# Kernel tuning notes

Hardware: AMD Instinct MI355X
Metric: run time of the kernel (lower is better)

The kernel has to match this reference:

```python
import jax, jax.numpy as jnp
import numpy as np

B, L, D = 16, 2048, 256

def setup_inputs() -> dict:
    key = jax.random.key(0)
    k1, k2 = jax.random.split(key)
    inp = jax.random.normal(k1, (B, L, D), dtype=jnp.float32)
    # Linear(2*dim, 1, bias=False) weight, torch layout [out=1, in=2*dim]
    v_w = jax.random.normal(k2, (1, 2 * D), dtype=jnp.float32) * (1.0 / np.sqrt(2 * D))
    return {"inp": inp, "v_w": v_w}


def reference(inp, v_w):
    # score[b,i,j] = cat(query=inp[b,i], key=inp[b,j]) . v_w
    # decomposes exactly into two rank-1 projections broadcast-summed.
    dim = inp.shape[-1]
    wq = v_w[0, :dim]   # multiplies the query half (unsqueeze(1) -> index i)
    wk = v_w[0, dim:]   # multiplies the key half (unsqueeze(2) -> index j)
    sq = jnp.einsum('bld,d->bl', inp, wq)          # [B,L]
    sk = jnp.einsum('bld,d->bl', inp, wk)          # [B,L]
    score = sq[:, :, None] + sk[:, None, :]        # [B,L,L]
    attn = jax.nn.softmax(score, axis=2)           # Softmax(2)
    out = jnp.einsum('bij,bjd->bid', attn, inp)    # bmm
    return (out, attn)
```

## Files before the change

kernel.cpp:

```cpp
#include <hip/hip_runtime.h>

#define BB 16
#define LL 2048
#define DD 256

__global__ void k1_sk(const float* __restrict__ inp, const float* __restrict__ wk,
                      float* __restrict__ sk) {
    int tid  = threadIdx.x;
    int wid  = tid >> 6, lane = tid & 63;
    int row  = blockIdx.x * 4 + wid;
    const float4 a = *reinterpret_cast<const float4*>(inp + (size_t)row * DD + lane * 4);
    const float4 w = *reinterpret_cast<const float4*>(wk + lane * 4);
    float dot = a.x * w.x + a.y * w.y + a.z * w.z + a.w * w.w;
    #pragma unroll
    for (int off = 32; off >= 1; off >>= 1) dot += __shfl_down(dot, off, 64);
    if (lane == 0) sk[row] = dot;
}

__global__ void k2_softmax(const float* __restrict__ sk, float* __restrict__ p) {
    int b = blockIdx.x;
    int tid = threadIdx.x;
    int lane = tid & 63, wid = tid >> 6;
    const float* skb = sk + b * LL;
    float v[8];
    #pragma unroll
    for (int r = 0; r < 8; ++r) v[r] = skb[tid + r * 256];
    float mx = v[0];
    #pragma unroll
    for (int r = 1; r < 8; ++r) mx = fmaxf(mx, v[r]);
    __shared__ float sm[4];
    __shared__ float bc;
    #pragma unroll
    for (int off = 32; off >= 1; off >>= 1) mx = fmaxf(mx, __shfl_down(mx, off, 64));
    if (lane == 0) sm[wid] = mx;
    __syncthreads();
    if (tid == 0) bc = fmaxf(fmaxf(sm[0], sm[1]), fmaxf(sm[2], sm[3]));
    __syncthreads();
    float m = bc;
    float e[8], s = 0.f;
    #pragma unroll
    for (int r = 0; r < 8; ++r) { e[r] = __expf(v[r] - m); s += e[r]; }
    #pragma unroll
    for (int off = 32; off >= 1; off >>= 1) s += __shfl_down(s, off, 64);
    __syncthreads();
    if (lane == 0) sm[wid] = s;
    __syncthreads();
    if (tid == 0) bc = (sm[0] + sm[1]) + (sm[2] + sm[3]);
    __syncthreads();
    float inv = 1.0f / bc;
    #pragma unroll
    for (int r = 0; r < 8; ++r) p[b * LL + tid + r * 256] = e[r] * inv;
}

__global__ void k3a_partial(const float* __restrict__ inp, const float* __restrict__ p,
                            float* __restrict__ partial) {
    int blk = blockIdx.x;
    int b = blk >> 4, jc = blk & 15;
    int t = threadIdx.x;
    const float* pb = p + b * LL + jc * 128;
    const float* ib = inp + ((size_t)(b * LL + jc * 128)) * DD + t;
    float acc = 0.f;
    #pragma unroll 4
    for (int j = 0; j < 128; ++j) acc += pb[j] * ib[(size_t)j * DD];
    partial[(size_t)blk * DD + t] = acc;
}

__global__ void k3b_reduce(const float* __restrict__ partial, float* __restrict__ out_vec) {
    int b = blockIdx.x;
    int t = threadIdx.x;
    float acc = 0.f;
    #pragma unroll
    for (int jc = 0; jc < 16; ++jc) acc += partial[((size_t)(b * 16 + jc)) * DD + t];
    out_vec[b * DD + t] = acc;
}

__global__ void k4_write(const float4* __restrict__ outv4, const float4* __restrict__ p4,
                         float4* __restrict__ dst) {
    const size_t OUT4 = (size_t)BB * LL * DD / 4;
    const size_t TOT4 = OUT4 + (size_t)BB * LL * LL / 4;
    size_t stride = (size_t)gridDim.x * blockDim.x;
    for (size_t i = blockIdx.x * (size_t)blockDim.x + threadIdx.x; i < TOT4; i += stride) {
        float4 v;
        if (i < OUT4) {
            size_t b  = i >> 17;
            size_t d4 = i & 63;
            v = outv4[(b << 6) + d4];
        } else {
            size_t k  = i - OUT4;
            size_t b  = k >> 20;
            size_t j4 = k & 511;
            v = p4[(b << 9) + j4];
        }
        dst[i] = v;
    }
}

extern "C" void kernel_launch(void* const* d_in, const int* in_sizes, int n_in,
                              void* d_out, int out_size, void* d_ws, size_t ws_size,
                              hipStream_t stream) {
    const float* inp = (const float*)d_in[0];
    const float* vw  = (const float*)d_in[1];
    float* out = (float*)d_out;
    float* ws  = (float*)d_ws;

    float* sk      = ws;
    float* p       = ws + 32768;
    float* partial = ws + 65536;
    float* out_vec = ws + 131072;

    k1_sk      <<<8192, 256, 0, stream>>>(inp, vw + DD, sk);
    k2_softmax <<<BB,   256, 0, stream>>>(sk, p);
    k3a_partial<<<256,  256, 0, stream>>>(inp, p, partial);
    k3b_reduce <<<BB,   256, 0, stream>>>(partial, out_vec);
    k4_write   <<<2048, 256, 0, stream>>>((const float4*)out_vec, (const float4*)p,
                                          (float4*)out);
}
```

Before: 80.49 us.

## Overlap attention broadcast writes with weighted-sum partials in one split kernel

Merges the partial weighted-sum kernel and the large attention-matrix broadcast write into one launch. The first 128 blocks compute per-segment partial sums while the remaining blocks stream the softmax row into the attention output with nontemporal stores. The final kernel reduces the partials and writes the broadcast output rows directly, which removes the separate reduce kernel and the out_vec round trip. The cost is fewer, longer-running partial blocks, and the nontemporal stores may behave differently on this cache hierarchy.

```diff
diff --git a/kernel.cpp b/kernel.cpp
--- a/kernel.cpp
+++ b/kernel.cpp
@@ -3,6 +3,11 @@
 #define BB 16
 #define LL 2048
 #define DD 256
+#define PB 128
+#define K3BLK 2048
+#define K3WR (K3BLK - PB)
+
+typedef float vf4 __attribute__((ext_vector_type(4)));
 
 __global__ void k1_sk(const float* __restrict__ inp, const float* __restrict__ wk,
                       float* __restrict__ sk) {
@@ -52,46 +57,45 @@
     for (int r = 0; r < 8; ++r) p[b * LL + tid + r * 256] = e[r] * inv;
 }
 
-__global__ void k3a_partial(const float* __restrict__ inp, const float* __restrict__ p,
-                            float* __restrict__ partial) {
-    int blk = blockIdx.x;
-    int b = blk >> 4, jc = blk & 15;
-    int t = threadIdx.x;
-    const float* pb = p + b * LL + jc * 128;
-    const float* ib = inp + ((size_t)(b * LL + jc * 128)) * DD + t;
-    float acc = 0.f;
-    #pragma unroll 4
-    for (int j = 0; j < 128; ++j) acc += pb[j] * ib[(size_t)j * DD];
-    partial[(size_t)blk * DD + t] = acc;
+__global__ void k3_split(const float* __restrict__ inp, const float* __restrict__ p,
+                         float* __restrict__ partial, float* __restrict__ out) {
+    const int blk = blockIdx.x, t = threadIdx.x;
+    const size_t OUT4 = (size_t)BB * LL * DD / 4;
+    const size_t ATT4 = (size_t)BB * LL * LL / 4;
+    if (blk < PB) {
+        int b = blk >> 3, seg = blk & 7;
+        const float* pb = p + b * LL + seg * 256;
+        const float* ib = inp + ((size_t)(b * LL + seg * 256)) * DD + t;
+        float acc = 0.f;
+        #pragma unroll 8
+        for (int j = 0; j < 256; ++j) acc += pb[j] * ib[(size_t)j * DD];
+        partial[blk * DD + t] = acc;
+    } else {
+        vf4* dst4 = (vf4*)out + OUT4;
+        const vf4* p4 = (const vf4*)p;
+        const size_t stride = (size_t)K3WR * 256;
+        for (size_t k = (size_t)(blk - PB) * 256 + t; k < ATT4; k += stride) {
+            size_t b = k >> 20, j4 = k & 511;
+            __builtin_nontemporal_store(p4[(b << 9) + j4], &dst4[k]);
+        }
+    }
 }
 
-__global__ void k3b_reduce(const float* __restrict__ partial, float* __restrict__ out_vec) {
-    int b = blockIdx.x;
-    int t = threadIdx.x;
+__global__ void k4_out(const float* __restrict__ partial, float* __restrict__ out) {
+    const int blk = blockIdx.x, t = threadIdx.x;
+    const int b = blk >> 4;
     float acc = 0.f;
     #pragma unroll
-    for (int jc = 0; jc < 16; ++jc) acc += partial[((size_t)(b * 16 + jc)) * DD + t];
-    out_vec[b * DD + t] = acc;
-}
-
-__global__ void k4_write(const float4* __restrict__ outv4, const float4* __restrict__ p4,
-                         float4* __restrict__ dst) {
-    const size_t OUT4 = (size_t)BB * LL * DD / 4;
-    const size_t TOT4 = OUT4 + (size_t)BB * LL * LL / 4;
-    size_t stride = (size_t)gridDim.x * blockDim.x;
-    for (size_t i = blockIdx.x * (size_t)blockDim.x + threadIdx.x; i < TOT4; i += stride) {
-        float4 v;
-        if (i < OUT4) {
-            size_t b  = i >> 17;
-            size_t d4 = i & 63;
-            v = outv4[(b << 6) + d4];
-        } else {
-            size_t k  = i - OUT4;
-            size_t b  = k >> 20;
-            size_t j4 = k & 511;
-            v = p4[(b << 9) + j4];
-        }
-        dst[i] = v;
+    for (int seg = 0; seg < 8; ++seg) acc += partial[(b * 8 + seg) * DD + t];
+    __shared__ float ov[DD];
+    ov[t] = acc;
+    __syncthreads();
+    const vf4* ovv = (const vf4*)ov;
+    vf4* dst = (vf4*)out + (size_t)blk * 8192;
+    #pragma unroll 4
+    for (int it = 0; it < 32; ++it) {
+        int idx = it * 256 + t;
+        __builtin_nontemporal_store(ovv[idx & 63], &dst[idx]);
     }
 }
 
@@ -106,12 +110,9 @@
     float* sk      = ws;
     float* p       = ws + 32768;
     float* partial = ws + 65536;
-    float* out_vec = ws + 131072;
 
     k1_sk      <<<8192, 256, 0, stream>>>(inp, vw + DD, sk);
     k2_softmax <<<BB,   256, 0, stream>>>(sk, p);
-    k3a_partial<<<256,  256, 0, stream>>>(inp, p, partial);
-    k3b_reduce <<<BB,   256, 0, stream>>>(partial, out_vec);
-    k4_write   <<<2048, 256, 0, stream>>>((const float4*)out_vec, (const float4*)p,
-                                          (float4*)out);
+    k3_split   <<<K3BLK,256, 0, stream>>>(inp, p, partial, out);
+    k4_out     <<<256,  256, 0, stream>>>(partial, out);
 }
```

Measured after the change: 67.20 us. -16.5%, faster.
